# Kernel tuning notes

Measured on AMD Instinct MI355X. Metric: run time of the kernel, lower is better.

Reference implementation:

```python
import jax, jax.numpy as jnp
import numpy as np

B, C, N, K, G = 4, 128, 4096, 9, 4


def setup_inputs() -> dict:
    key = jax.random.key(0)
    ks = jax.random.split(key, 4)
    s = 0.05
    return {
        "features": jax.random.normal(ks[0], (B, C, N, 1), jnp.float32),
        # Attn.linear: Conv2d(2C -> C, 1x1)
        "w_lin": jax.random.normal(ks[1], (C, 2 * C), jnp.float32) * s,
        "b_lin": jnp.zeros((C,), jnp.float32),
        # atten_weight_conv: Linear(C -> K*G)
        "w_aw": jax.random.normal(ks[2], (K * G, C), jnp.float32) * s,
        "b_aw": jnp.zeros((K * G,), jnp.float32),
        # GroupNorm(4, C)
        "gn_g": jnp.ones((C,), jnp.float32),
        "gn_b": jnp.zeros((C,), jnp.float32),
        # conv: Conv2d(C -> C, 1x1) + BatchNorm2d(C)
        "conv_w": jax.random.normal(ks[3], (C, C), jnp.float32) * s,
        "conv_b": jnp.zeros((C,), jnp.float32),
        "bn_g": jnp.ones((C,), jnp.float32),
        "bn_b": jnp.zeros((C,), jnp.float32),
    }


def reference(features, w_lin, b_lin, w_aw, b_aw, gn_g, gn_b, conv_w, conv_b, bn_g, bn_b):
    B, C, N, _ = features.shape
    K, G = 9, 4
    Cg = C // G  # 32 channels per group
    EPS = 1e-5

    x = features[..., 0]                       # [B,C,N]
    # ---- KNN graph (negative squared distance, top-k) ----
    xx = jnp.sum(x * x, axis=1)                # [B,N]
    inner = jnp.einsum('bcn,bcm->bnm', x, x)   # [B,N,N]
    pd = 2.0 * inner - xx[:, :, None] - xx[:, None, :]
    idx = jax.lax.top_k(pd, K)[1]              # [B,N,K]

    # ---- edge feature gather: cat(x, x - x_neighbor) ----
    xt = x.transpose(0, 2, 1)                  # [B,N,C]
    b_ix = jnp.arange(B)[:, None, None]
    nbr = xt[b_ix, idx]                        # [B,N,K,C]
    ctr = jnp.broadcast_to(xt[:, :, None, :], (B, N, K, C))
    edge = jnp.concatenate([ctr, ctr - nbr], axis=-1)   # [B,N,K,2C]

    # ---- Attn.linear (1x1 conv == per-position linear) ----
    feat = jnp.einsum('bnke,ce->bnkc', edge, w_lin) + b_lin  # [B,N,K,C]

    # ---- grouped channel attention (4 groups of 32) ----
    fg = feat.reshape(B, N, K, G, Cg)
    scores = jnp.einsum('bnkgc,bnjgc->bngkj', fg, fg) / np.sqrt(32.0)
    s = jax.nn.softmax(scores, axis=-1)        # [B,N,G,K,K]
    attn = jnp.einsum('bngkj,bnjgc->bngkc', s, jax.nn.elu(fg))  # [B,N,G,K,Cg]

    # ---- attention weights over neighbors ----
    aw = jnp.einsum('bnc,dc->bnd', xt, w_aw) + b_aw          # [B,N,K*G]
    aw = jax.nn.softmax(aw.reshape(B, N, G, K), axis=-1)     # [B,N,G,K]

    # ---- weighted neighbor combine ----
    lf = jnp.einsum('bngk,bngkc->bngc', aw, attn)            # [B,N,G,Cg]
    lf = lf.transpose(0, 2, 3, 1).reshape(B, C, N, 1)        # [B,C,N,1]

    # ---- GroupNorm(4, C) over residual ----
    y = lf + features
    yg = y.reshape(B, G, Cg * N)
    mu = yg.mean(-1, keepdims=True)
    var = yg.var(-1, keepdims=True)
    yn = ((yg - mu) / jnp.sqrt(var + EPS)).reshape(B, C, N, 1)
    yn = yn * gn_g[None, :, None, None] + gn_b[None, :, None, None]

    # ---- 1x1 conv + BatchNorm (training-mode batch stats) + ReLU ----
    z = jnp.einsum('oc,bcnk->bonk', conv_w, yn) + conv_b[None, :, None, None]
    m = z.mean(axis=(0, 2, 3), keepdims=True)
    v = z.var(axis=(0, 2, 3), keepdims=True)
    z = (z - m) / jnp.sqrt(v + EPS) * bn_g[None, :, None, None] + bn_b[None, :, None, None]
    return jax.nn.relu(z)
```

## Files before the change

### kernel.cpp

```cpp
#include <hip/hip_runtime.h>
#include <hip/hip_bf16.h>
#include <cstddef>

#define NPTS 4096
#define CCH  128
#define KNN  9
#define GRP  4
#define BB   4
#define OFF_XT    0u
#define OFF_XX    2097152u
#define OFF_XHI   2113536u
#define OFF_IDX   3162112u
#define OFF_O     3309568u
#define OFF_Y     8159232u
#define OFF_GNP   10256384u
#define OFF_GNA   10387456u
#define OFF_GND   10387968u
#define OFF_WP    10388480u
#define OFF_BIASP 10454016u
#define OFF_BNSUM 10454528u
#define OFF_BNSQ  10454656u
#define OFF_BNSC  10454784u
#define OFF_BNSH  10454912u

using bf16x8 = __attribute__((ext_vector_type(8))) short;
using f32x4  = __attribute__((ext_vector_type(4))) float;

#define CE(a, b) { float _h = fmaxf(a, b); b = fminf(a, b); a = _h; }

#define SENT_BITS 0xFF7FF000u

__global__ void k_transpose(const float* __restrict__ x, float* __restrict__ xt,
                            __hip_bfloat16* __restrict__ xhi, float* __restrict__ xx) {
  __shared__ float t[32][33];
  int tx = threadIdx.x, ty = threadIdx.y;
  int n0 = blockIdx.x * 32, c0 = blockIdx.y * 32, b = blockIdx.z;
  float v = x[((size_t)b * CCH + c0 + ty) * NPTS + n0 + tx];
  t[ty][tx] = v;
  __syncthreads();
  float tv = t[tx][ty];
  size_t R = (size_t)b * NPTS + n0 + ty;
  int c = c0 + tx;
  xt[R * CCH + c] = tv;
  int g = c >> 3, w = c & 7;
  int sc = (((g ^ ((n0 + ty) & 15)) << 3) | w);
  xhi[R * CCH + sc] = __float2bfloat16(tv);
  if (ty == 0) {
    float s = 0.f;
    #pragma unroll
    for (int k = 0; k < 32; k++) { float u = t[k][tx]; s += u * u; }
    atomicAdd(&xx[b * NPTS + n0 + tx], s);
  }
}

__device__ __forceinline__ void select_chunk(int c, int wave, int quad,
                                             const f32x4 (&acc)[2][2],
                                             float (&top8)[2][8]) {
  const unsigned cbase = (unsigned)(c * 128 + wave * 32 + quad * 4);
  #pragma unroll
  for (int qt = 0; qt < 2; qt++) {
    float k[8];
    #pragma unroll
    for (int ct = 0; ct < 2; ct++)
      #pragma unroll
      for (int r = 0; r < 4; r++) {
        unsigned u = __float_as_uint(acc[ct][qt][r]);
        k[ct * 4 + r] = __uint_as_float((u & 0xFFFFF000u) |
                                        (cbase + (unsigned)(ct * 16 + r)));
      }
    CE(k[0],k[1]) CE(k[2],k[3]) CE(k[4],k[5]) CE(k[6],k[7])
    CE(k[0],k[2]) CE(k[1],k[3]) CE(k[4],k[6]) CE(k[5],k[7])
    CE(k[1],k[2]) CE(k[5],k[6])
    CE(k[0],k[4]) CE(k[1],k[5]) CE(k[2],k[6]) CE(k[3],k[7])
    CE(k[2],k[4]) CE(k[3],k[5])
    CE(k[1],k[2]) CE(k[3],k[4]) CE(k[5],k[6])
    float t[8];
    #pragma unroll
    for (int i = 0; i < 8; i++) t[i] = fmaxf(top8[qt][i], k[7 - i]);
    CE(t[0],t[4]) CE(t[1],t[5]) CE(t[2],t[6]) CE(t[3],t[7])
    CE(t[0],t[2]) CE(t[1],t[3]) CE(t[4],t[6]) CE(t[5],t[7])
    CE(t[0],t[1]) CE(t[2],t[3]) CE(t[4],t[5]) CE(t[6],t[7])
    #pragma unroll
    for (int i = 0; i < 8; i++) top8[qt][i] = t[i];
  }
}

__device__ __forceinline__ void load_chunk(const short* __restrict__ xb,
                                           const int (&aoff)[2][4], int c,
                                           bf16x8 (&af)[2][4]) {
  const short* cb = xb + c * (128 * CCH);
  #pragma unroll
  for (int ct = 0; ct < 2; ct++)
    #pragma unroll
    for (int ks = 0; ks < 4; ks++)
      af[ct][ks] = *(const bf16x8*)(cb + aoff[ct][ks]);
}

__device__ __forceinline__ void load_cinit(const float* __restrict__ xxb, int base, int c,
                                           f32x4 (&ci)[2]) {
  #pragma unroll
  for (int ct = 0; ct < 2; ct++)
    #pragma unroll
    for (int r = 0; r < 4; r++)
      ci[ct][r] = -0.5f * xxb[c * 128 + base + ct * 16 + r];
}

__device__ __forceinline__ void mfma_chunk(const bf16x8 (&af)[2][4],
                                           const bf16x8 (&qf)[2][4],
                                           const f32x4 (&ci)[2], f32x4 (&acc)[2][2]) {
  #pragma unroll
  for (int ct = 0; ct < 2; ct++)
    #pragma unroll
    for (int qt = 0; qt < 2; qt++) acc[ct][qt] = ci[ct];
  #pragma unroll
  for (int ks = 0; ks < 4; ks++)
    #pragma unroll
    for (int ct = 0; ct < 2; ct++)
      #pragma unroll
      for (int qt = 0; qt < 2; qt++)
        acc[ct][qt] = __builtin_amdgcn_mfma_f32_16x16x32_bf16(
            af[ct][ks], qf[qt][ks], acc[ct][qt], 0, 0, 0);
}

__launch_bounds__(256, 2)
__global__ void k_knn(const short* __restrict__ xhi, const float* __restrict__ xx,
                      float* __restrict__ cand) {
  const int tid = threadIdx.x;
  const int wave = tid >> 6, lane = tid & 63;
  const int quad = lane >> 4, m = lane & 15;
  const int b = blockIdx.y;
  const int q0 = blockIdx.x * 32;
  const short* xb = xhi + (size_t)b * NPTS * CCH;
  const float* xxb = xx + (b << 12);
  const int base = wave * 32 + quad * 4;

  bf16x8 qfrag[2][4];
  #pragma unroll
  for (int qt = 0; qt < 2; qt++) {
    const short* qrow = xb + (size_t)(q0 + qt * 16 + m) * CCH;
    #pragma unroll
    for (int ks = 0; ks < 4; ks++) {
      int slot = (ks * 4 + quad) ^ m;
      qfrag[qt][ks] = *(const bf16x8*)(qrow + slot * 8);
    }
  }

  int aoff[2][4];
  #pragma unroll
  for (int ct = 0; ct < 2; ct++)
    #pragma unroll
    for (int ks = 0; ks < 4; ks++)
      aoff[ct][ks] = (wave * 32 + ct * 16 + m) * CCH + (((ks * 4 + quad) ^ m) * 8);

  float top8[2][8];
  #pragma unroll
  for (int qt = 0; qt < 2; qt++)
    #pragma unroll
    for (int p = 0; p < 8; p++) top8[qt][p] = __uint_as_float(SENT_BITS);

  f32x4 acc[2][2];
  bf16x8 bufA[2][4], bufB[2][4];
  f32x4 ciA[2], ciB[2];

  load_chunk(xb, aoff, 0, bufA);
  load_cinit(xxb, base, 0, ciA);

  for (int c = 0; c < 32; c += 2) {
    load_chunk(xb, aoff, c + 1, bufB);
    load_cinit(xxb, base, c + 1, ciB);
    if (c > 0) select_chunk(c - 1, wave, quad, acc, top8);
    mfma_chunk(bufA, qfrag, ciA, acc);
    if (c + 2 < 32) {
      load_chunk(xb, aoff, c + 2, bufA);
      load_cinit(xxb, base, c + 2, ciA);
    }
    select_chunk(c, wave, quad, acc, top8);
    mfma_chunk(bufB, qfrag, ciB, acc);
  }
  select_chunk(31, wave, quad, acc, top8);

  int slot = wave * 4 + quad;
  #pragma unroll
  for (int qt = 0; qt < 2; qt++) {
    int q = q0 + qt * 16 + m;
    float* dst = cand + ((size_t)((b << 12) + q) * 16 + slot) * 8;
    #pragma unroll
    for (int p = 0; p < 8; p++) dst[p] = top8[qt][p];
  }
}

__launch_bounds__(256)
__global__ void k_rerank(const float* __restrict__ cand, const float* __restrict__ xt,
                         const float* __restrict__ xx, int* __restrict__ idxOut) {
  __shared__ __align__(16) float arr[4][128];
  __shared__ int selS[4][16];
  __shared__ float keyS[4][16];
  int tid = threadIdx.x, wave = tid >> 6, lane = tid & 63;
  int qg = blockIdx.x * 4 + wave;
  int b = qg >> 12;
  const float* src = cand + (size_t)qg * 128;
  float e1 = src[lane], e2 = src[lane + 64];
  arr[wave][lane] = e1; arr[wave][lane + 64] = e2;
  __syncthreads();
  int r1 = 0, r2 = 0;
  #pragma unroll 8
  for (int f = 0; f < 128; f += 4) {
    float4 fv = *(const float4*)&arr[wave][f];
    r1 += (fv.x > e1) + (fv.y > e1) + (fv.z > e1) + (fv.w > e1);
    r2 += (fv.x > e2) + (fv.y > e2) + (fv.z > e2) + (fv.w > e2);
  }
  if (r1 < 16) selS[wave][r1] = (int)(__float_as_uint(e1) & 0xFFFu);
  if (r2 < 16) selS[wave][r2] = (int)(__float_as_uint(e2) & 0xFFFu);
  __syncthreads();
  int cnum = lane >> 2, part = lane & 3;
  int cidx = selS[wave][cnum];
  const float* rq = xt + (size_t)qg * CCH;
  const float* rc = xt + ((size_t)(b << 12) + cidx) * CCH;
  float dot = 0.f;
  #pragma unroll
  for (int j = 0; j < 8; j++) {
    float4 a4 = *(const float4*)&rq[part * 32 + j * 4];
    float4 c4 = *(const float4*)&rc[part * 32 + j * 4];
    dot += a4.x * c4.x + a4.y * c4.y + a4.z * c4.z + a4.w * c4.w;
  }
  dot += __shfl_xor(dot, 1);
  dot += __shfl_xor(dot, 2);
  if (part == 0)
    keyS[wave][cnum] = fmaf(2.f, dot, -xx[(b << 12) + cidx]);
  __syncthreads();
  if (lane < 16) {
    float k = keyS[wave][lane]; int i = selS[wave][lane];
    int r = 0;
    #pragma unroll
    for (int f = 0; f < 16; f++) {
      float fk = keyS[wave][f]; int fi = selS[wave][f];
      r += (fk > k) || (fk == k && fi < i);
    }
    if (r < 9) idxOut[(size_t)qg * 9 + r] = i;
  }
}

__launch_bounds__(256)
__global__ void k_linear(const float* __restrict__ xt, const float* __restrict__ w_lin,
                         const float* __restrict__ b_lin, const float* __restrict__ w_aw,
                         const float* __restrict__ b_aw, float* __restrict__ O) {
  __shared__ __align__(16) float Xs[64 * 132];
  __shared__ __align__(16) float Ws[64 * 132];
  int tid = threadIdx.x;
  int tx = tid & 15, ty = tid >> 4;
  int p0 = blockIdx.x * 64, o0 = blockIdx.y * 64;
  #pragma unroll
  for (int i = 0; i < 8; i++) {
    int flat = tid + i * 256; int r = flat >> 5, c4 = flat & 31;
    *(float4*)&Xs[r * 132 + c4 * 4] = *(const float4*)&xt[(size_t)(p0 + r) * CCH + c4 * 4];
  }
  #pragma unroll
  for (int i = 0; i < 8; i++) {
    int flat = tid + i * 256; int r = flat >> 5, c4 = flat & 31;
    int o = o0 + r; float4 v;
    if (o < 128) {
      float4 a = *(const float4*)&w_lin[(size_t)o * 256 + c4 * 4];
      float4 c = *(const float4*)&w_lin[(size_t)o * 256 + 128 + c4 * 4];
      v = make_float4(a.x + c.x, a.y + c.y, a.z + c.z, a.w + c.w);
    } else if (o < 256) {
      v = *(const float4*)&w_lin[(size_t)(o - 128) * 256 + 128 + c4 * 4];
    } else if (o < 292) {
      v = *(const float4*)&w_aw[(size_t)(o - 256) * 128 + c4 * 4];
    } else v = make_float4(0.f, 0.f, 0.f, 0.f);
    *(float4*)&Ws[r * 132 + c4 * 4] = v;
  }
  __syncthreads();
  float acc[4][4] = {};
  #pragma unroll 2
  for (int kq = 0; kq < 32; kq++) {
    float4 xa[4], wb[4];
    #pragma unroll
    for (int i = 0; i < 4; i++) xa[i] = *(const float4*)&Xs[(ty * 4 + i) * 132 + kq * 4];
    #pragma unroll
    for (int j = 0; j < 4; j++) wb[j] = *(const float4*)&Ws[(tx + 16 * j) * 132 + kq * 4];
    #pragma unroll
    for (int i = 0; i < 4; i++)
      #pragma unroll
      for (int j = 0; j < 4; j++)
        acc[i][j] += xa[i].x * wb[j].x + xa[i].y * wb[j].y + xa[i].z * wb[j].z + xa[i].w * wb[j].w;
  }
  #pragma unroll
  for (int j = 0; j < 4; j++) {
    int o = o0 + tx + 16 * j;
    if (o < 292) {
      float bias = (o < 128) ? b_lin[o] : ((o < 256) ? 0.f : b_aw[o - 256]);
      #pragma unroll
      for (int i = 0; i < 4; i++)
        O[(size_t)(p0 + ty * 4 + i) * 296 + o] = acc[i][j] + bias;
    }
  }
}

__launch_bounds__(256)
__global__ void k_attn(const float* __restrict__ O, const int* __restrict__ idxArr,
                       const float* __restrict__ xt, float* __restrict__ Y,
                       float* __restrict__ gnPart) {
  __shared__ __align__(16) float fF[4][1188];
  __shared__ __align__(16) float scS[4][432];
  __shared__ float awS[4][48];
  __shared__ float w9S[4][48];
  __shared__ int tI[45], tJ[45];
  int tid = threadIdx.x;
  int wave = tid >> 6, l = tid & 63;
  int pos = blockIdx.x * 4 + wave;
  int b = pos >> 12;
  if (tid == 0) {
    int p = 0;
    for (int i = 0; i < 9; i++) for (int j = i; j < 9; j++) { tI[p] = i; tJ[p] = j; p++; }
  }
  int nbr[9];
  const float* Op = O + (size_t)pos * 296;
  #pragma unroll
  for (int k = 0; k < 9; k++) nbr[k] = idxArr[(size_t)pos * 9 + k];
  float2 u = *(const float2*)(Op + 2 * l);
  float* fFw = fF[wave];
  #pragma unroll
  for (int k = 0; k < 9; k++) {
    const float* vp = O + (size_t)((b << 12) + nbr[k]) * 296 + 128;
    float2 vv = *(const float2*)(vp + 2 * l);
    *(float2*)&fFw[k * 132 + 2 * l] = make_float2(u.x - vv.x, u.y - vv.y);
  }
  __syncthreads();
  #pragma unroll
  for (int r = 0; r < 3; r++) {
    int p = r * 64 + l;
    if (p < 180) {
      int g = p / 45, q = p - g * 45;
      int i = tI[q], j = tJ[q];
      const float* fi = fFw + i * 132 + g * 32;
      const float* fj = fFw + j * 132 + g * 32;
      float s = 0.f;
      #pragma unroll
      for (int t8 = 0; t8 < 8; t8++) {
        float4 a4 = *(const float4*)(fi + 4 * t8);
        float4 b4 = *(const float4*)(fj + 4 * t8);
        s += a4.x * b4.x + a4.y * b4.y + a4.z * b4.z + a4.w * b4.w;
      }
      s *= 0.17677669529663687f;
      scS[wave][(g * 9 + i) * 12 + j] = s;
      scS[wave][(g * 9 + j) * 12 + i] = s;
    }
  }
  __syncthreads();
  if (l < 36) {
    int g = l / 9, i = l - g * 9;
    float* rp = &scS[wave][(g * 9 + i) * 12];
    float mx = rp[0];
    #pragma unroll
    for (int j = 1; j < 9; j++) mx = fmaxf(mx, rp[j]);
    float e[9]; float sm = 0.f;
    #pragma unroll
    for (int j = 0; j < 9; j++) { e[j] = __expf(rp[j] - mx); sm += e[j]; }
    float inv = 1.f / sm;
    #pragma unroll
    for (int j = 0; j < 9; j++) rp[j] = e[j] * inv;
  } else if (l < 40) {
    int g = l - 36;
    float a[9]; float mx = -3.4e38f;
    #pragma unroll
    for (int k = 0; k < 9; k++) { a[k] = Op[256 + g * 9 + k]; mx = fmaxf(mx, a[k]); }
    float sm = 0.f;
    #pragma unroll
    for (int k = 0; k < 9; k++) { a[k] = __expf(a[k] - mx); sm += a[k]; }
    float inv = 1.f / sm;
    #pragma unroll
    for (int k = 0; k < 9; k++) awS[wave][g * 12 + k] = a[k] * inv;
  }
  __syncthreads();
  if (l < 36) {
    int g = l / 9, j = l - g * 9;
    float s = 0.f;
    #pragma unroll
    for (int i = 0; i < 9; i++) s += awS[wave][g * 12 + i] * scS[wave][(g * 9 + i) * 12 + j];
    w9S[wave][g * 12 + j] = s;
  }
  __syncthreads();
  int g = l >> 4;
  float w9r[9];
  #pragma unroll
  for (int j = 0; j < 9; j++) w9r[j] = w9S[wave][g * 12 + j];
  int c0 = 2 * l;
  float lf0 = 0.f, lf1 = 0.f;
  #pragma unroll
  for (int j = 0; j < 9; j++) {
    float2 f2 = *(const float2*)&fFw[j * 132 + c0];
    float e0 = f2.x > 0.f ? f2.x : __expf(f2.x) - 1.f;
    float e1 = f2.y > 0.f ? f2.y : __expf(f2.y) - 1.f;
    lf0 += w9r[j] * e0;
    lf1 += w9r[j] * e1;
  }
  float2 xv = *(const float2*)(xt + (size_t)pos * CCH + c0);
  float y0 = lf0 + xv.x, y1 = lf1 + xv.y;
  *(float2*)(Y + (size_t)pos * CCH + c0) = make_float2(y0, y1);
  float s1 = y0 + y1, s2 = y0 * y0 + y1 * y1;
  #pragma unroll
  for (int mm = 1; mm <= 8; mm <<= 1) { s1 += __shfl_xor(s1, mm); s2 += __shfl_xor(s2, mm); }
  if ((l & 15) == 0) {
    gnPart[(size_t)pos * 8 + g * 2]     = s1;
    gnPart[(size_t)pos * 8 + g * 2 + 1] = s2;
  }
}

__global__ void k_gnstats(const float* __restrict__ gnPart,
                          const float* __restrict__ gn_g, const float* __restrict__ gn_b,
                          float* __restrict__ gnA, float* __restrict__ gnD) {
  int bg = blockIdx.x; int b = bg >> 2, g = bg & 3;
  int tid = threadIdx.x;
  float s1 = 0.f, s2 = 0.f;
  for (int r = tid; r < NPTS; r += 256) {
    const float* p = gnPart + (size_t)(b * NPTS + r) * 8 + g * 2;
    s1 += p[0]; s2 += p[1];
  }
  __shared__ float r1[256], r2[256];
  r1[tid] = s1; r2[tid] = s2;
  __syncthreads();
  for (int off = 128; off > 0; off >>= 1) {
    if (tid < off) { r1[tid] += r1[tid + off]; r2[tid] += r2[tid + off]; }
    __syncthreads();
  }
  __shared__ float muS, rsS;
  if (tid == 0) {
    float mu = r1[0] * (1.f / 131072.f);
    float var = r2[0] * (1.f / 131072.f) - mu * mu;
    muS = mu; rsS = 1.f / sqrtf(var + 1e-5f);
  }
  __syncthreads();
  if (tid < 32) {
    int c = g * 32 + tid;
    float a = rsS * gn_g[c];
    gnA[b * 128 + c] = a;
    gnD[b * 128 + c] = gn_b[c] - muS * a;
  }
}

__global__ void k_fold(const float* __restrict__ conv_w, const float* __restrict__ conv_b,
                       const float* __restrict__ gnA, const float* __restrict__ gnD,
                       float* __restrict__ Wp, float* __restrict__ biasp) {
  int b = blockIdx.x; int tid = threadIdx.x;
  __shared__ float dS[128], aS[128];
  if (tid < 128) { dS[tid] = gnD[b * 128 + tid]; aS[tid] = gnA[b * 128 + tid]; }
  __syncthreads();
  for (int f = tid; f < 16384; f += 256)
    Wp[(size_t)b * 16384 + f] = conv_w[f] * aS[f & 127];
  if (tid < 128) {
    float s = conv_b[tid];
    for (int c = 0; c < 128; c++) s += conv_w[tid * 128 + c] * dS[c];
    biasp[b * 128 + tid] = s;
  }
}

__launch_bounds__(256)
__global__ void k_conv(const float* __restrict__ Y, const float* __restrict__ Wp,
                       const float* __restrict__ biasp, float* __restrict__ zpre,
                       float* __restrict__ bnSum, float* __restrict__ bnSq) {
  __shared__ __align__(16) float Ys[64 * 132];
  __shared__ __align__(16) float Ws[64 * 132];
  int tid = threadIdx.x;
  int tx = tid & 15, ty = tid >> 4;
  int n0 = blockIdx.x * 64, o0 = blockIdx.y * 64, b = blockIdx.z;
  #pragma unroll
  for (int i = 0; i < 8; i++) {
    int flat = tid + i * 256; int r = flat >> 5, c4 = flat & 31;
    *(float4*)&Ys[r * 132 + c4 * 4] = *(const float4*)&Y[(size_t)((b << 12) + n0 + r) * CCH + c4 * 4];
    *(float4*)&Ws[r * 132 + c4 * 4] = *(const float4*)&Wp[(size_t)b * 16384 + (size_t)(o0 + r) * 128 + c4 * 4];
  }
  __syncthreads();
  float acc[4][4] = {};
  #pragma unroll 2
  for (int kq = 0; kq < 32; kq++) {
    float4 wa[4], yb[4];
    #pragma unroll
    for (int i = 0; i < 4; i++) wa[i] = *(const float4*)&Ws[(ty * 4 + i) * 132 + kq * 4];
    #pragma unroll
    for (int j = 0; j < 4; j++) yb[j] = *(const float4*)&Ys[(tx + 16 * j) * 132 + kq * 4];
    #pragma unroll
    for (int i = 0; i < 4; i++)
      #pragma unroll
      for (int j = 0; j < 4; j++)
        acc[i][j] += wa[i].x * yb[j].x + wa[i].y * yb[j].y + wa[i].z * yb[j].z + wa[i].w * yb[j].w;
  }
  #pragma unroll
  for (int i = 0; i < 4; i++) {
    int o = o0 + ty * 4 + i;
    float bias = biasp[b * 128 + o];
    float p1 = 0.f, p2 = 0.f;
    #pragma unroll
    for (int j = 0; j < 4; j++) {
      float z = acc[i][j] + bias;
      zpre[(((size_t)((b << 7) + o)) << 12) + n0 + tx + 16 * j] = z;
      p1 += z; p2 += z * z;
    }
    #pragma unroll
    for (int mm = 1; mm <= 8; mm <<= 1) { p1 += __shfl_xor(p1, mm); p2 += __shfl_xor(p2, mm); }
    if (tx == 0) { atomicAdd(&bnSum[o], p1); atomicAdd(&bnSq[o], p2); }
  }
}

__global__ void k_bnfin(const float* __restrict__ bnSum, const float* __restrict__ bnSq,
                        const float* __restrict__ bn_g, const float* __restrict__ bn_b,
                        float* __restrict__ bnScale, float* __restrict__ bnShift) {
  int o = threadIdx.x;
  float m = bnSum[o] * (1.f / 16384.f);
  float v = bnSq[o] * (1.f / 16384.f) - m * m;
  float sc = bn_g[o] / sqrtf(v + 1e-5f);
  bnScale[o] = sc;
  bnShift[o] = bn_b[o] - m * sc;
}

__global__ void k_final(const float* __restrict__ zpre, const float* __restrict__ bnScale,
                        const float* __restrict__ bnShift, float* __restrict__ out) {
  int i4 = blockIdx.x * 256 + threadIdx.x;
  int e = i4 * 4;
  int o = (e >> 12) & 127;
  float4 z = *(const float4*)&zpre[e];
  float sc = bnScale[o], sh = bnShift[o];
  float4 r;
  r.x = fmaxf(fmaf(z.x, sc, sh), 0.f);
  r.y = fmaxf(fmaf(z.y, sc, sh), 0.f);
  r.z = fmaxf(fmaf(z.z, sc, sh), 0.f);
  r.w = fmaxf(fmaf(z.w, sc, sh), 0.f);
  *(float4*)&out[e] = r;
}

extern "C" void kernel_launch(void* const* d_in, const int* in_sizes, int n_in,
                              void* d_out, int out_size, void* d_ws, size_t ws_size,
                              hipStream_t stream) {
  const float* features = (const float*)d_in[0];
  const float* w_lin  = (const float*)d_in[1];
  const float* b_lin  = (const float*)d_in[2];
  const float* w_aw   = (const float*)d_in[3];
  const float* b_aw   = (const float*)d_in[4];
  const float* gn_g   = (const float*)d_in[5];
  const float* gn_b   = (const float*)d_in[6];
  const float* conv_w = (const float*)d_in[7];
  const float* conv_b = (const float*)d_in[8];
  const float* bn_g   = (const float*)d_in[9];
  const float* bn_b   = (const float*)d_in[10];

  float* ws    = (float*)d_ws;
  float* xt    = ws + OFF_XT;
  float* xxp   = ws + OFF_XX;
  __hip_bfloat16* xhip = (__hip_bfloat16*)(ws + OFF_XHI);
  int*   idxp  = (int*)(ws + OFF_IDX);
  float* Op    = ws + OFF_O;
  float* candp = ws + OFF_O;
  float* Yp    = ws + OFF_Y;
  float* gnp   = ws + OFF_GNP;
  float* gnA   = ws + OFF_GNA;
  float* gnD   = ws + OFF_GND;
  float* Wp    = ws + OFF_WP;
  float* biasp = ws + OFF_BIASP;
  float* bnSum = ws + OFF_BNSUM;
  float* bnSq  = ws + OFF_BNSQ;
  float* bnSc  = ws + OFF_BNSC;
  float* bnSh  = ws + OFF_BNSH;
  float* zpre  = xt;

  hipMemsetAsync(xxp, 0, NPTS * BB * sizeof(float), stream);
  hipMemsetAsync(bnSum, 0, 256 * sizeof(float), stream);

  k_transpose<<<dim3(128, 4, 4), dim3(32, 32), 0, stream>>>(features, xt, xhip, xxp);
  k_knn<<<dim3(128, 4), 256, 0, stream>>>((const short*)xhip, xxp, candp);
  k_rerank<<<4096, 256, 0, stream>>>(candp, xt, xxp, idxp);
  k_linear<<<dim3(256, 5), 256, 0, stream>>>(xt, w_lin, b_lin, w_aw, b_aw, Op);
  k_attn<<<4096, 256, 0, stream>>>(Op, idxp, xt, Yp, gnp);
  k_gnstats<<<16, 256, 0, stream>>>(gnp, gn_g, gn_b, gnA, gnD);
  k_fold<<<4, 256, 0, stream>>>(conv_w, conv_b, gnA, gnD, Wp, biasp);
  k_conv<<<dim3(64, 2, 4), 256, 0, stream>>>(Yp, Wp, biasp, zpre, bnSum, bnSq);
  k_bnfin<<<1, 128, 0, stream>>>(bnSum, bnSq, bn_g, bn_b, bnSc, bnSh);
  k_final<<<2048, 256, 0, stream>>>(zpre, bnSc, bnSh, (float*)d_out);
}
```

Before: 275.5 us.

## Split KNN candidate scan across two grid halves and merge via bitonic max

The KNN kernel's candidate-column loop is split in two along a new grid z dimension, doubling the block count from 512 to 1024 so the 256-CU device is better filled. Each half writes its own per-slot top-8 lists. The rerank kernel merges the two halves with an elementwise max of one list against the reversed other, which acts as a bitonic merge step. Launch bounds are raised to 4 blocks per SM, which tightens the register budget and may cause spills. The merge depends on the top-8 lists being sorted and on the candidate buffer fitting twice as many entries.

```diff
diff --git a/kernel.cpp b/kernel.cpp
--- a/kernel.cpp
+++ b/kernel.cpp
@@ -122,7 +122,7 @@
             af[ct][ks], qf[qt][ks], acc[ct][qt], 0, 0, 0);
 }
 
-__launch_bounds__(256, 2)
+__launch_bounds__(256, 4)
 __global__ void k_knn(const short* __restrict__ xhi, const float* __restrict__ xx,
                       float* __restrict__ cand) {
   const int tid = threadIdx.x;
@@ -130,6 +130,7 @@
   const int quad = lane >> 4, m = lane & 15;
   const int b = blockIdx.y;
   const int q0 = blockIdx.x * 32;
+  const int ch0 = blockIdx.z * 16;
   const short* xb = xhi + (size_t)b * NPTS * CCH;
   const float* xxb = xx + (b << 12);
   const int base = wave * 32 + quad * 4;
@@ -162,28 +163,28 @@
   bf16x8 bufA[2][4], bufB[2][4];
   f32x4 ciA[2], ciB[2];
 
-  load_chunk(xb, aoff, 0, bufA);
-  load_cinit(xxb, base, 0, ciA);
-
-  for (int c = 0; c < 32; c += 2) {
+  load_chunk(xb, aoff, ch0, bufA);
+  load_cinit(xxb, base, ch0, ciA);
+
+  for (int c = ch0; c < ch0 + 16; c += 2) {
     load_chunk(xb, aoff, c + 1, bufB);
     load_cinit(xxb, base, c + 1, ciB);
-    if (c > 0) select_chunk(c - 1, wave, quad, acc, top8);
+    if (c > ch0) select_chunk(c - 1, wave, quad, acc, top8);
     mfma_chunk(bufA, qfrag, ciA, acc);
-    if (c + 2 < 32) {
+    if (c + 2 < ch0 + 16) {
       load_chunk(xb, aoff, c + 2, bufA);
       load_cinit(xxb, base, c + 2, ciA);
     }
     select_chunk(c, wave, quad, acc, top8);
     mfma_chunk(bufB, qfrag, ciB, acc);
   }
-  select_chunk(31, wave, quad, acc, top8);
+  select_chunk(ch0 + 15, wave, quad, acc, top8);
 
   int slot = wave * 4 + quad;
   #pragma unroll
   for (int qt = 0; qt < 2; qt++) {
     int q = q0 + qt * 16 + m;
-    float* dst = cand + ((size_t)((b << 12) + q) * 16 + slot) * 8;
+    float* dst = cand + ((size_t)((b << 12) + q) * 32 + blockIdx.z * 16 + slot) * 8;
     #pragma unroll
     for (int p = 0; p < 8; p++) dst[p] = top8[qt][p];
   }
@@ -198,10 +199,23 @@
   int tid = threadIdx.x, wave = tid >> 6, lane = tid & 63;
   int qg = blockIdx.x * 4 + wave;
   int b = qg >> 12;
-  const float* src = cand + (size_t)qg * 128;
-  float e1 = src[lane], e2 = src[lane + 64];
-  arr[wave][lane] = e1; arr[wave][lane + 64] = e2;
-  __syncthreads();
+  const float* src = cand + (size_t)qg * 256;
+  if (lane < 16) {
+    float4 a0 = *(const float4*)&src[lane * 8];
+    float4 a1 = *(const float4*)&src[lane * 8 + 4];
+    float4 b0 = *(const float4*)&src[128 + lane * 8];
+    float4 b1 = *(const float4*)&src[128 + lane * 8 + 4];
+    arr[wave][lane * 8 + 0] = fmaxf(a0.x, b1.w);
+    arr[wave][lane * 8 + 1] = fmaxf(a0.y, b1.z);
+    arr[wave][lane * 8 + 2] = fmaxf(a0.z, b1.y);
+    arr[wave][lane * 8 + 3] = fmaxf(a0.w, b1.x);
+    arr[wave][lane * 8 + 4] = fmaxf(a1.x, b0.w);
+    arr[wave][lane * 8 + 5] = fmaxf(a1.y, b0.z);
+    arr[wave][lane * 8 + 6] = fmaxf(a1.z, b0.y);
+    arr[wave][lane * 8 + 7] = fmaxf(a1.w, b0.x);
+  }
+  __syncthreads();
+  float e1 = arr[wave][lane], e2 = arr[wave][lane + 64];
   int r1 = 0, r2 = 0;
   #pragma unroll 8
   for (int f = 0; f < 128; f += 4) {
@@ -565,7 +579,7 @@
   hipMemsetAsync(bnSum, 0, 256 * sizeof(float), stream);
 
   k_transpose<<<dim3(128, 4, 4), dim3(32, 32), 0, stream>>>(features, xt, xhip, xxp);
-  k_knn<<<dim3(128, 4), 256, 0, stream>>>((const short*)xhip, xxp, candp);
+  k_knn<<<dim3(128, 4, 2), 256, 0, stream>>>((const short*)xhip, xxp, candp);
   k_rerank<<<4096, 256, 0, stream>>>(candp, xt, xxp, idxp);
   k_linear<<<dim3(256, 5), 256, 0, stream>>>(xt, w_lin, b_lin, w_aw, b_aw, Op);
   k_attn<<<4096, 256, 0, stream>>>(Op, idxp, xt, Yp, gnp);
```

New measurement: 347.0 us. 26.0% more time.
